# Kernel optimization log

Measured on AMD Instinct MI355X. Metric: run time of the kernel, lower is better.

## Reference

```python
import jax, jax.numpy as jnp
import numpy as np

B, F, T, D, W = 65536, 8, 60, 10, 6  # batch, features, time, window, n_windows
EPS = 1e-8
BN_EPS = 1e-5
IU, JU = np.triu_indices(F, k=1)  # 28 feature pairs


def _bn1d(x, g, b):
    # training-mode BatchNorm1d over [B, C, L]: stats over (B, L) per channel
    m = x.mean(axis=(0, 2), keepdims=True)
    v = x.var(axis=(0, 2), keepdims=True)
    return (x - m) * jax.lax.rsqrt(v + BN_EPS) * g[None, :, None] + b[None, :, None]


def setup_inputs() -> dict:
    key = jax.random.key(0)
    ks = jax.random.split(key, 8)
    s = 0.1
    return {
        "xb": jax.random.normal(ks[0], (B, 1, F, T), dtype=jnp.float32),
        "conv_w": jax.random.normal(ks[1], (4, 1, 1, D), dtype=jnp.float32) * s,
        "conv_b": jnp.zeros((4,), jnp.float32),
        "bn1_g": jnp.ones((28,), jnp.float32), "bn1_b": jnp.zeros((28,), jnp.float32),
        "bn4_g": jnp.ones((F,), jnp.float32), "bn4_b": jnp.zeros((F,), jnp.float32),
        "bn6_g": jnp.ones((F,), jnp.float32), "bn6_b": jnp.zeros((F,), jnp.float32),
        "bn9_g": jnp.ones((32,), jnp.float32), "bn9_b": jnp.zeros((32,), jnp.float32),
        "bnmax_g": jnp.ones((76,), jnp.float32), "bnmax_b": jnp.zeros((76,), jnp.float32),
        "w1": jax.random.normal(ks[2], (30, 608), dtype=jnp.float32) * s,
        "b1": jnp.zeros((30,), jnp.float32),
        "w2": jax.random.normal(ks[3], (1, 30), dtype=jnp.float32) * s,
        "b2": jnp.zeros((1,), jnp.float32),
    }


def reference(xb, conv_w, conv_b, bn1_g, bn1_b, bn4_g, bn4_b, bn6_g, bn6_b,
              bn9_g, bn9_b, bnmax_g, bnmax_b, w1, b1, w2, b2):
    b = xb.shape[0]
    xw = xb.reshape(b, F, W, D)  # non-overlapping windows of length D=10

    # ts_corr: pairwise Pearson correlation per window -> [b, 28, W]
    mu = xw.mean(axis=-1, keepdims=True)
    c = xw - mu
    cov = jnp.einsum('bfwt,bgwt->bfgw', c, c) / D          # [b,F,F,W]
    std = jnp.sqrt((c * c).mean(axis=-1) + EPS)            # [b,F,W]
    corr = cov / (std[:, :, None, :] * std[:, None, :, :] + EPS)
    xb1 = corr[:, IU, JU, :]                               # [b,28,W]

    # ts_zscore: mean/std per window -> [b, F, W]
    xb4 = mu[..., 0] / (std + EPS)

    # ts_decaylinear: linear-decay weighted mean -> [b, F, W]
    dw = jnp.arange(1, D + 1, dtype=jnp.float32)
    dw = dw / dw.sum()
    xb6 = jnp.einsum('bfwt,t->bfw', xw, dw)

    # conv2d kernel (1,10) stride (1,10) -> [b, 4*F, W]
    xb9 = jnp.einsum('bfwt,ot->bofw', xw, conv_w[:, 0, 0, :]) + conv_b[None, :, None, None]
    xb9 = xb9.reshape(b, 4 * F, W)

    h = jnp.concatenate([
        _bn1d(xb1, bn1_g, bn1_b),
        _bn1d(xb4, bn4_g, bn4_b),
        _bn1d(xb6, bn6_g, bn6_b),
        _bn1d(xb9, bn9_g, bn9_b),
    ], axis=1)                                             # [b,76,6]

    h_max = h.reshape(b, 76, 2, 3).max(axis=-1)            # MaxPool1d(3,3) -> [b,76,2]
    h_max = _bn1d(h_max, bnmax_g, bnmax_b)

    flat = jnp.concatenate([h.reshape(b, -1), h_max.reshape(b, -1)], axis=1)  # [b,608]
    out = jax.nn.relu(flat @ w1.T + b1) @ w2.T + b2
    return out.reshape(-1)
```

## Files before the change

kernel.cpp:

```cpp
#include <hip/hip_runtime.h>


#define NB 65536
#define EPS_F    1e-8f
#define BN_EPS_F 1e-5f

__device__ __forceinline__ float frcp(float x) {
  return __builtin_amdgcn_rcpf(x);
}

template<int Ctrl, int RowMask>
__device__ __forceinline__ float dpp_mov0(float v) {
  return __int_as_float(__builtin_amdgcn_update_dpp(
      0, __float_as_int(v), Ctrl, RowMask, 0xf, true));
}
__device__ __forceinline__ float wave_sum64(float v) {
  v += dpp_mov0<0x111, 0xf>(v);
  v += dpp_mov0<0x112, 0xf>(v);
  v += dpp_mov0<0x114, 0xf>(v);
  v += dpp_mov0<0x118, 0xf>(v);
  v += dpp_mov0<0x142, 0xa>(v);
  v += dpp_mov0<0x143, 0xc>(v);
  return v;
}

__host__ __device__ constexpr int UT(int i, int j) { return i*8 - i*(i-1)/2 + (j - i); }
__host__ __device__ constexpr int PIDX(int i, int j) { return i*7 - i*(i-1)/2 + (j - i - 1); }


__global__ void __launch_bounds__(256, 4)
k1f(const float* __restrict__ xb, const float* __restrict__ cw,
    const float* __restrict__ cb, float* __restrict__ F) {
  const int tid  = threadIdx.x;
  const int wave = tid >> 6, lane = tid & 63;
  const int role = __builtin_amdgcn_readfirstlane(wave);
  const int h    = role & 1;
  const int s    = blockIdx.x * 64 + lane;
  const float* xrow = xb + (size_t)s * 480 + h * 30;

  if (role < 2) {
    float mA[28];
    #pragma unroll
    for (int p = 0; p < 28; ++p) mA[p] = -3.0e38f;
    #pragma unroll
    for (int wl = 0; wl < 3; ++wl) {
      float sum[8], S[36];
      #pragma unroll
      for (int f = 0; f < 8; ++f) sum[f] = 0.f;
      #pragma unroll
      for (int k = 0; k < 36; ++k) S[k] = 0.f;
      #pragma unroll
      for (int tp = 0; tp < 5; ++tp) {
        float2 x2[8];
        #pragma unroll
        for (int f = 0; f < 8; ++f)
          x2[f] = *reinterpret_cast<const float2*>(xrow + f*60 + wl*10 + tp*2);
        #pragma unroll
        for (int f = 0; f < 8; ++f) sum[f] += x2[f].x + x2[f].y;
        #pragma unroll
        for (int i = 0; i < 8; ++i)
          #pragma unroll
          for (int j = i; j < 8; ++j)
            S[UT(i,j)] = fmaf(x2[i].y, x2[j].y, fmaf(x2[i].x, x2[j].x, S[UT(i,j)]));
      }
      float mu[8], sd[8];
      #pragma unroll
      for (int f = 0; f < 8; ++f) {
        mu[f] = sum[f] * 0.1f;
        sd[f] = sqrtf(fmaf(-mu[f], mu[f], S[UT(f,f)] * 0.1f) + EPS_F);
      }
      #pragma unroll
      for (int i = 0; i < 8; ++i)
        #pragma unroll
        for (int j = i + 1; j < 8; ++j) {
          float cov = fmaf(-mu[i], mu[j], S[UT(i,j)] * 0.1f);
          float v = cov * frcp(fmaf(sd[i], sd[j], EPS_F));
          int p = PIDX(i,j);
          F[(size_t)(p*6 + h*3 + wl) * NB + s] = v;
          mA[p] = fmaxf(mA[p], v);
        }
    }
    #pragma unroll
    for (int p = 0; p < 28; ++p)
      F[(size_t)(456 + p*2 + h) * NB + s] = mA[p];
  } else {
    #pragma unroll 1
    for (int f = 0; f < 8; ++f) {
      float m6[6];
      #pragma unroll
      for (int k = 0; k < 6; ++k) m6[k] = -3.0e38f;
      #pragma unroll
      for (int wl = 0; wl < 3; ++wl) {
        float2 x2[5];
        #pragma unroll
        for (int tp = 0; tp < 5; ++tp)
          x2[tp] = *reinterpret_cast<const float2*>(xrow + f*60 + wl*10 + tp*2);
        float sm = 0.f, sq = 0.f, wsm = 0.f;
        #pragma unroll
        for (int tp = 0; tp < 5; ++tp) {
          sm += x2[tp].x + x2[tp].y;
          sq = fmaf(x2[tp].x, x2[tp].x, fmaf(x2[tp].y, x2[tp].y, sq));
          wsm = fmaf(x2[tp].x, (float)(2*tp+1) * (1.f/55.f),
                fmaf(x2[tp].y, (float)(2*tp+2) * (1.f/55.f), wsm));
        }
        float mu = sm * 0.1f;
        float sd = sqrtf(fmaf(-mu, mu, sq * 0.1f) + EPS_F);
        float vv[6];
        vv[0] = mu * frcp(sd + EPS_F);
        vv[1] = wsm;
        #pragma unroll
        for (int o = 0; o < 4; ++o) {
          float cv = cb[o];
          #pragma unroll
          for (int tp = 0; tp < 5; ++tp)
            cv = fmaf(x2[tp].x, cw[o*10 + 2*tp], fmaf(x2[tp].y, cw[o*10 + 2*tp + 1], cv));
          vv[2+o] = cv;
        }
        #pragma unroll
        for (int k = 0; k < 6; ++k) {
          m6[k] = fmaxf(m6[k], vv[k]);
          int ch = (k == 0) ? (28 + f) : (k == 1) ? (36 + f) : (44 + (k-2)*8 + f);
          F[(size_t)(ch*6 + h*3 + wl) * NB + s] = vv[k];
        }
      }
      #pragma unroll
      for (int k = 0; k < 6; ++k) {
        int ch = (k == 0) ? (28 + f) : (k == 1) ? (36 + f) : (44 + (k-2)*8 + f);
        F[(size_t)(456 + ch*2 + h) * NB + s] = m6[k];
      }
    }
  }
}

__global__ void __launch_bounds__(256, 4)
kS(const float* __restrict__ F, float* __restrict__ stats) {
  const int r     = blockIdx.x >> 1;
  const int chunk = blockIdx.x & 1;
  const float* p  = F + (size_t)r * NB + chunk * 32768;
  const int tid = threadIdx.x;
  const int wave = tid >> 6, lane = tid & 63;
  float s = 0.f, q = 0.f;
  #pragma unroll 8
  for (int i = 0; i < 32; ++i) {
    float4 v = *reinterpret_cast<const float4*>(p + (size_t)(i*256 + tid) * 4);
    s += (v.x + v.y) + (v.z + v.w);
    q = fmaf(v.x, v.x, fmaf(v.y, v.y, fmaf(v.z, v.z, fmaf(v.w, v.w, q))));
  }
  s = wave_sum64(s);
  q = wave_sum64(q);
  __shared__ float ls[4], lq[4];
  if (lane == 63) { ls[wave] = s; lq[wave] = q; }
  __syncthreads();
  if (tid == 0) {
    float ts = (ls[0] + ls[1]) + (ls[2] + ls[3]);
    float tq = (lq[0] + lq[1]) + (lq[2] + lq[3]);
    int si, qi;
    if (r < 456) { int c = r / 6;        si = c;       qi = 76 + c;  }
    else         { int c = (r - 456)>>1; si = 152 + c; qi = 228 + c; }
    atomicAdd(&stats[si], ts);
    atomicAdd(&stats[qi], tq);
  }
}

__global__ void __launch_bounds__(256, 4)
k3f(const float* __restrict__ F, const float* __restrict__ w1s,
    const float* __restrict__ c0, const float* __restrict__ w2,
    const float* __restrict__ b2, float* __restrict__ out) {
  const int tid  = threadIdx.x;
  const int wave = tid >> 6, lane = tid & 63;
  const int kq   = __builtin_amdgcn_readfirstlane(wave);
  const int s    = blockIdx.x * 64 + lane;

  float a[30];
  #pragma unroll
  for (int j = 0; j < 30; ++j) a[j] = 0.f;

  const float* fp = F + (size_t)(kq * 152) * NB + s;
  #pragma unroll 8
  for (int r = 0; r < 152; ++r) {
    float v = fp[(size_t)r * NB];
    const float* wr = w1s + (kq * 152 + r) * 30;
    #pragma unroll
    for (int j = 0; j < 30; ++j) a[j] = fmaf(v, wr[j], a[j]);
  }

  __shared__ float accA[4][64][31];
  #pragma unroll
  for (int j = 0; j < 30; ++j) accA[wave][lane][j] = a[j];
  __syncthreads();
  if (wave == 0) {
    float t = b2[0];
    #pragma unroll
    for (int j = 0; j < 30; ++j) {
      float hj = ((accA[0][lane][j] + accA[1][lane][j]) +
                  (accA[2][lane][j] + accA[3][lane][j])) + c0[j];
      t = fmaf(w2[j], fmaxf(hj, 0.f), t);
    }
    out[blockIdx.x * 64 + lane] = t;
  }
}


__global__ void k2_params(const float* __restrict__ stats,
    const float* __restrict__ bn1g, const float* __restrict__ bn1b,
    const float* __restrict__ bn4g, const float* __restrict__ bn4b,
    const float* __restrict__ bn6g, const float* __restrict__ bn6b,
    const float* __restrict__ bn9g, const float* __restrict__ bn9b,
    const float* __restrict__ bnmg, const float* __restrict__ bnmb,
    float* __restrict__ params) {
  int c = threadIdx.x;
  if (c >= 76) return;
  float g, b;
  if      (c < 28) { g = bn1g[c];    b = bn1b[c];    }
  else if (c < 36) { g = bn4g[c-28]; b = bn4b[c-28]; }
  else if (c < 44) { g = bn6g[c-36]; b = bn6b[c-36]; }
  else             { g = bn9g[c-44]; b = bn9b[c-44]; }
  const float in1 = 1.0f / (65536.0f * 6.0f);
  const float in2 = 1.0f / (65536.0f * 2.0f);
  float mean = stats[c] * in1;
  float var  = stats[76 + c] * in1 - mean * mean;
  float r    = rsqrtf(var + BN_EPS_F);
  float sc1  = g * r;
  float sh1  = b - mean * sc1;
  float mmr  = stats[152 + c] * in2;
  float vmr  = stats[228 + c] * in2 - mmr * mmr;
  float meanm = sc1 * mmr + sh1;
  float varm  = sc1 * sc1 * vmr;
  float rm  = rsqrtf(varm + BN_EPS_F);
  float scm = bnmg[c] * rm;
  float shm = bnmb[c] - meanm * scm;
  params[c]        = sc1;
  params[76 + c]   = sh1;
  params[152 + c]  = scm;
  params[228 + c]  = shm;
}

__global__ void k2b(const float* __restrict__ w1, const float* __restrict__ params,
                    const float* __restrict__ b1, float* __restrict__ w1s,
                    float* __restrict__ c0) {
  int r = blockIdx.x;
  int j = threadIdx.x;
  float sc, cst;
  if (r < 456) {
    int c = r / 6;
    sc = params[c]; cst = params[76 + c];
  } else {
    int c = (r - 456) >> 1;
    float sc1 = params[c], sh1 = params[76 + c];
    float scm = params[152 + c], shm = params[228 + c];
    sc = sc1 * scm; cst = fmaf(scm, sh1, shm);
  }
  if (j < 30) {
    float w = w1[j * 608 + r];
    w1s[r * 30 + j] = sc * w;
    float cadd = cst * w;
    if (r == 0) cadd += b1[j];
    atomicAdd(&c0[j], cadd);
  }
}


__device__ __forceinline__ void flush4(float* acc, int ch, float s, float q,
                                       float m, bool ll) {
  float t0 = wave_sum64(s);
  float t1 = wave_sum64(q);
  float t2 = wave_sum64(m);
  float t3 = wave_sum64(m * m);
  if (ll) {
    atomicAdd(&acc[ch], t0);
    atomicAdd(&acc[76 + ch], t1);
    atomicAdd(&acc[152 + ch], t2);
    atomicAdd(&acc[228 + ch], t3);
  }
}

__global__ void __launch_bounds__(256, 2)
k1_stats(const float* __restrict__ xb, const float* __restrict__ cw,
         const float* __restrict__ cb, float* __restrict__ stats) {
  const int tid  = threadIdx.x;
  const int wave = tid >> 6, lane = tid & 63;
  const int half = __builtin_amdgcn_readfirstlane(wave & 1);
  const int sl   = (wave >> 1) * 64 + lane;
  const int sample = blockIdx.x * 128 + sl;
  const float* xrow = xb + (size_t)sample * 480 + half * 30;
  const bool ll = (lane == 63);

  __shared__ float acc[304];
  for (int i = tid; i < 304; i += 256) acc[i] = 0.f;
  __syncthreads();

  {
    float sA[28], qA[28], mA[28];
    #pragma unroll
    for (int p = 0; p < 28; ++p) { sA[p] = 0.f; qA[p] = 0.f; mA[p] = -3.0e38f; }
    #pragma unroll
    for (int wl = 0; wl < 3; ++wl) {
      float sum[8], S[36];
      #pragma unroll
      for (int f = 0; f < 8; ++f) sum[f] = 0.f;
      #pragma unroll
      for (int k = 0; k < 36; ++k) S[k] = 0.f;
      #pragma unroll
      for (int tp = 0; tp < 5; ++tp) {
        float2 x2[8];
        #pragma unroll
        for (int f = 0; f < 8; ++f)
          x2[f] = *reinterpret_cast<const float2*>(xrow + f*60 + wl*10 + tp*2);
        #pragma unroll
        for (int f = 0; f < 8; ++f) sum[f] += x2[f].x + x2[f].y;
        #pragma unroll
        for (int i = 0; i < 8; ++i)
          #pragma unroll
          for (int j = i; j < 8; ++j)
            S[UT(i,j)] = fmaf(x2[i].y, x2[j].y, fmaf(x2[i].x, x2[j].x, S[UT(i,j)]));
      }
      float mu[8], sd[8];
      #pragma unroll
      for (int f = 0; f < 8; ++f) {
        mu[f] = sum[f] * 0.1f;
        sd[f] = sqrtf(fmaf(-mu[f], mu[f], S[UT(f,f)] * 0.1f) + EPS_F);
      }
      #pragma unroll
      for (int i = 0; i < 8; ++i)
        #pragma unroll
        for (int j = i + 1; j < 8; ++j) {
          float cov = fmaf(-mu[i], mu[j], S[UT(i,j)] * 0.1f);
          float v = cov * frcp(fmaf(sd[i], sd[j], EPS_F));
          int p = PIDX(i,j);
          sA[p] += v; qA[p] = fmaf(v, v, qA[p]); mA[p] = fmaxf(mA[p], v);
        }
    }
    #pragma unroll
    for (int p = 0; p < 28; ++p) flush4(acc, p, sA[p], qA[p], mA[p], ll);
  }

  #pragma unroll 1
  for (int f = 0; f < 8; ++f) {
    float s6[6], q6[6], m6[6];
    #pragma unroll
    for (int k = 0; k < 6; ++k) { s6[k] = 0.f; q6[k] = 0.f; m6[k] = -3.0e38f; }
    #pragma unroll
    for (int wl = 0; wl < 3; ++wl) {
      float2 x2[5];
      #pragma unroll
      for (int tp = 0; tp < 5; ++tp)
        x2[tp] = *reinterpret_cast<const float2*>(xrow + f*60 + wl*10 + tp*2);
      float sm = 0.f, sq = 0.f, wsm = 0.f;
      #pragma unroll
      for (int tp = 0; tp < 5; ++tp) {
        sm += x2[tp].x + x2[tp].y;
        sq = fmaf(x2[tp].x, x2[tp].x, fmaf(x2[tp].y, x2[tp].y, sq));
        wsm = fmaf(x2[tp].x, (float)(2*tp+1) * (1.f/55.f),
              fmaf(x2[tp].y, (float)(2*tp+2) * (1.f/55.f), wsm));
      }
      float mu = sm * 0.1f;
      float sd = sqrtf(fmaf(-mu, mu, sq * 0.1f) + EPS_F);
      float v0 = mu * frcp(sd + EPS_F);
      s6[0] += v0; q6[0] = fmaf(v0, v0, q6[0]); m6[0] = fmaxf(m6[0], v0);
      s6[1] += wsm; q6[1] = fmaf(wsm, wsm, q6[1]); m6[1] = fmaxf(m6[1], wsm);
      #pragma unroll
      for (int o = 0; o < 4; ++o) {
        float cv = cb[o];
        #pragma unroll
        for (int tp = 0; tp < 5; ++tp)
          cv = fmaf(x2[tp].x, cw[o*10 + 2*tp], fmaf(x2[tp].y, cw[o*10 + 2*tp + 1], cv));
        s6[2+o] += cv; q6[2+o] = fmaf(cv, cv, q6[2+o]); m6[2+o] = fmaxf(m6[2+o], cv);
      }
    }
    flush4(acc, 28 + f, s6[0], q6[0], m6[0], ll);
    flush4(acc, 36 + f, s6[1], q6[1], m6[1], ll);
    #pragma unroll
    for (int o = 0; o < 4; ++o)
      flush4(acc, 44 + o*8 + f, s6[2+o], q6[2+o], m6[2+o], ll);
  }

  __syncthreads();
  for (int i = tid; i < 304; i += 256) atomicAdd(&stats[i], acc[i]);
}

__global__ void __launch_bounds__(256, 2)
k3_out(const float* __restrict__ xb, const float* __restrict__ cw,
       const float* __restrict__ cb, const float* __restrict__ w1s,
       const float* __restrict__ c0, const float* __restrict__ w2,
       const float* __restrict__ b2, float* __restrict__ out) {
  const int tid  = threadIdx.x;
  const int wave = tid >> 6, lane = tid & 63;
  const int half = __builtin_amdgcn_readfirstlane(wave & 1);
  const int sl   = (wave >> 1) * 64 + lane;
  const int sample = blockIdx.x * 128 + sl;
  const float* xrow = xb + (size_t)sample * 480 + half * 30;

  float a[30];
  #pragma unroll
  for (int j = 0; j < 30; ++j) a[j] = 0.f;

  {
    float mA[28];
    #pragma unroll
    for (int p = 0; p < 28; ++p) mA[p] = -3.0e38f;
    #pragma unroll
    for (int wl = 0; wl < 3; ++wl) {
      float sum[8], S[36];
      #pragma unroll
      for (int f = 0; f < 8; ++f) sum[f] = 0.f;
      #pragma unroll
      for (int k = 0; k < 36; ++k) S[k] = 0.f;
      #pragma unroll
      for (int tp = 0; tp < 5; ++tp) {
        float2 x2[8];
        #pragma unroll
        for (int f = 0; f < 8; ++f)
          x2[f] = *reinterpret_cast<const float2*>(xrow + f*60 + wl*10 + tp*2);
        #pragma unroll
        for (int f = 0; f < 8; ++f) sum[f] += x2[f].x + x2[f].y;
        #pragma unroll
        for (int i = 0; i < 8; ++i)
          #pragma unroll
          for (int j = i; j < 8; ++j)
            S[UT(i,j)] = fmaf(x2[i].y, x2[j].y, fmaf(x2[i].x, x2[j].x, S[UT(i,j)]));
      }
      float mu[8], sd[8];
      #pragma unroll
      for (int f = 0; f < 8; ++f) {
        mu[f] = sum[f] * 0.1f;
        sd[f] = sqrtf(fmaf(-mu[f], mu[f], S[UT(f,f)] * 0.1f) + EPS_F);
      }
      #pragma unroll
      for (int i = 0; i < 8; ++i)
        #pragma unroll
        for (int j = i + 1; j < 8; ++j) {
          float cov = fmaf(-mu[i], mu[j], S[UT(i,j)] * 0.1f);
          float v = cov * frcp(fmaf(sd[i], sd[j], EPS_F));
          int p = PIDX(i,j);
          mA[p] = fmaxf(mA[p], v);
          const float* wr = w1s + (p*6 + half*3 + wl) * 30;
          #pragma unroll
          for (int j2 = 0; j2 < 30; ++j2) a[j2] = fmaf(v, wr[j2], a[j2]);
        }
    }
    #pragma unroll
    for (int p = 0; p < 28; ++p) {
      const float* wr = w1s + (456 + p*2 + half) * 30;
      #pragma unroll
      for (int j2 = 0; j2 < 30; ++j2) a[j2] = fmaf(mA[p], wr[j2], a[j2]);
    }
  }

  #pragma unroll 1
  for (int f = 0; f < 8; ++f) {
    float m6[6];
    #pragma unroll
    for (int k = 0; k < 6; ++k) m6[k] = -3.0e38f;
    #pragma unroll
    for (int wl = 0; wl < 3; ++wl) {
      float2 x2[5];
      #pragma unroll
      for (int tp = 0; tp < 5; ++tp)
        x2[tp] = *reinterpret_cast<const float2*>(xrow + f*60 + wl*10 + tp*2);
      float sm = 0.f, sq = 0.f, wsm = 0.f;
      #pragma unroll
      for (int tp = 0; tp < 5; ++tp) {
        sm += x2[tp].x + x2[tp].y;
        sq = fmaf(x2[tp].x, x2[tp].x, fmaf(x2[tp].y, x2[tp].y, sq));
        wsm = fmaf(x2[tp].x, (float)(2*tp+1) * (1.f/55.f),
              fmaf(x2[tp].y, (float)(2*tp+2) * (1.f/55.f), wsm));
      }
      float mu = sm * 0.1f;
      float sd = sqrtf(fmaf(-mu, mu, sq * 0.1f) + EPS_F);
      float vv[6];
      vv[0] = mu * frcp(sd + EPS_F);
      vv[1] = wsm;
      #pragma unroll
      for (int o = 0; o < 4; ++o) {
        float cv = cb[o];
        #pragma unroll
        for (int tp = 0; tp < 5; ++tp)
          cv = fmaf(x2[tp].x, cw[o*10 + 2*tp], fmaf(x2[tp].y, cw[o*10 + 2*tp + 1], cv));
        vv[2+o] = cv;
      }
      #pragma unroll
      for (int k = 0; k < 6; ++k) {
        m6[k] = fmaxf(m6[k], vv[k]);
        int ch = (k == 0) ? (28 + f) : (k == 1) ? (36 + f) : (44 + (k-2)*8 + f);
        const float* wr = w1s + (ch*6 + half*3 + wl) * 30;
        #pragma unroll
        for (int j2 = 0; j2 < 30; ++j2) a[j2] = fmaf(vv[k], wr[j2], a[j2]);
      }
    }
    #pragma unroll
    for (int k = 0; k < 6; ++k) {
      int ch = (k == 0) ? (28 + f) : (k == 1) ? (36 + f) : (44 + (k-2)*8 + f);
      const float* wr = w1s + (456 + ch*2 + half) * 30;
      #pragma unroll
      for (int j2 = 0; j2 < 30; ++j2) a[j2] = fmaf(m6[k], wr[j2], a[j2]);
    }
  }

  __shared__ float accA[128][31];
  if (half == 0) {
    #pragma unroll
    for (int j = 0; j < 30; ++j) accA[sl][j] = a[j];
  }
  __syncthreads();
  if (half == 1) {
    #pragma unroll
    for (int j = 0; j < 30; ++j) accA[sl][j] += a[j];
  }
  __syncthreads();
  if (tid < 128) {
    float t = b2[0];
    #pragma unroll
    for (int j = 0; j < 30; ++j)
      t = fmaf(w2[j], fmaxf(accA[tid][j] + c0[j], 0.f), t);
    out[blockIdx.x * 128 + tid] = t;
  }
}


extern "C" void kernel_launch(void* const* d_in, const int* in_sizes, int n_in,
                              void* d_out, int out_size, void* d_ws, size_t ws_size,
                              hipStream_t stream) {
  (void)in_sizes; (void)n_in; (void)out_size;
  const float* xb   = (const float*)d_in[0];
  const float* cw   = (const float*)d_in[1];
  const float* cb   = (const float*)d_in[2];
  const float* bn1g = (const float*)d_in[3];
  const float* bn1b = (const float*)d_in[4];
  const float* bn4g = (const float*)d_in[5];
  const float* bn4b = (const float*)d_in[6];
  const float* bn6g = (const float*)d_in[7];
  const float* bn6b = (const float*)d_in[8];
  const float* bn9g = (const float*)d_in[9];
  const float* bn9b = (const float*)d_in[10];
  const float* bnmg = (const float*)d_in[11];
  const float* bnmb = (const float*)d_in[12];
  const float* w1   = (const float*)d_in[13];
  const float* b1   = (const float*)d_in[14];
  const float* w2   = (const float*)d_in[15];
  const float* b2   = (const float*)d_in[16];

  float* out    = (float*)d_out;
  float* ws     = (float*)d_ws;
  float* stats  = ws;
  float* params = ws + 304;
  float* c0     = ws + 608;
  float* w1s    = ws + 640;
  float* F      = ws + 18880;

  const size_t needed = ((size_t)18880 + (size_t)608 * NB) * sizeof(float);

  hipMemsetAsync(ws, 0, 640 * sizeof(float), stream);
  if (ws_size >= needed) {
    k1f<<<1024, 256, 0, stream>>>(xb, cw, cb, F);
    kS<<<1216, 256, 0, stream>>>(F, stats);
    k2_params<<<1, 128, 0, stream>>>(stats, bn1g, bn1b, bn4g, bn4b, bn6g, bn6b,
                                     bn9g, bn9b, bnmg, bnmb, params);
    k2b<<<608, 64, 0, stream>>>(w1, params, b1, w1s, c0);
    k3f<<<1024, 256, 0, stream>>>(F, w1s, c0, w2, b2, out);
  } else {
    k1_stats<<<512, 256, 0, stream>>>(xb, cw, cb, stats);
    k2_params<<<1, 128, 0, stream>>>(stats, bn1g, bn1b, bn4g, bn4b, bn6g, bn6b,
                                     bn9g, bn9b, bnmg, bnmb, params);
    k2b<<<608, 64, 0, stream>>>(w1, params, b1, w1s, c0);
    k3_out<<<512, 256, 0, stream>>>(xb, cw, cb, w1s, c0, w2, b2, out);
  }
}
```

Before: 381.6 us.

## Replace materialized feature buffer with two-pass recompute kernels staging input in LDS

Removes the 608×B intermediate feature tensor and its separate stats-reduction kernel. Instead it runs one templated kernel twice: a first pass that recomputes features and accumulates BN statistics with wave reductions and atomics, and a second pass that recomputes features and applies the folded linear layer directly. Input tiles are loaded coalesced into LDS in two halves with register prefetch, and work is split across waves by feature groups. This trades DRAM traffic for duplicated feature computation and higher LDS and register usage.

```diff
diff --git a/kernel.cpp b/kernel.cpp
--- a/kernel.cpp
+++ b/kernel.cpp
@@ -4,6 +4,7 @@
 #define NB 65536
 #define EPS_F    1e-8f
 #define BN_EPS_F 1e-5f
+#define LDSW 242
 
 __device__ __forceinline__ float frcp(float x) {
   return __builtin_amdgcn_rcpf(x);
@@ -24,179 +25,282 @@
   return v;
 }
 
-__host__ __device__ constexpr int UT(int i, int j) { return i*8 - i*(i-1)/2 + (j - i); }
-__host__ __device__ constexpr int PIDX(int i, int j) { return i*7 - i*(i-1)/2 + (j - i - 1); }
-
-
-__global__ void __launch_bounds__(256, 4)
-k1f(const float* __restrict__ xb, const float* __restrict__ cw,
-    const float* __restrict__ cb, float* __restrict__ F) {
-  const int tid  = threadIdx.x;
-  const int wave = tid >> 6, lane = tid & 63;
-  const int role = __builtin_amdgcn_readfirstlane(wave);
-  const int h    = role & 1;
-  const int s    = blockIdx.x * 64 + lane;
-  const float* xrow = xb + (size_t)s * 480 + h * 30;
-
-  if (role < 2) {
-    float mA[28];
-    #pragma unroll
-    for (int p = 0; p < 28; ++p) mA[p] = -3.0e38f;
+constexpr int PI_[28] = {0,0,0,0,0,0,0, 1,1,1,1,1,1, 2,2,2,2,2, 3,3,3,3, 4,4,4, 5,5, 6};
+constexpr int PJ_[28] = {1,2,3,4,5,6,7, 2,3,4,5,6,7, 3,4,5,6,7, 4,5,6,7, 5,6,7, 6,7, 7};
+
+template<int PASS, int W>
+__device__ __forceinline__ void corr_wave(
+    const float* __restrict__ bx, const int h,
+    const float* __restrict__ w1s,
+    float* __restrict__ sacc, float* __restrict__ qacc,
+    float* __restrict__ msacc, float* __restrict__ m2acc,
+    float* __restrict__ a)
+{
+  constexpr int PLO = W * 14;
+  constexpr int FLO = W * 4;
+  float m[18];
+  #pragma unroll
+  for (int k = 0; k < 18; ++k) m[k] = -3.0e38f;
+
+  #pragma unroll
+  for (int wl = 0; wl < 3; ++wl) {
+    float sum[8], SD[8], SP[14];
+    #pragma unroll
+    for (int f = 0; f < 8; ++f) { sum[f] = 0.f; SD[f] = 0.f; }
+    #pragma unroll
+    for (int k = 0; k < 14; ++k) SP[k] = 0.f;
+    #pragma unroll
+    for (int tp = 0; tp < 5; ++tp) {
+      float2 x2[8];
+      #pragma unroll
+      for (int f = 0; f < 8; ++f)
+        x2[f] = *reinterpret_cast<const float2*>(bx + f*30 + wl*10 + tp*2);
+      #pragma unroll
+      for (int f = 0; f < 8; ++f) {
+        sum[f] += x2[f].x + x2[f].y;
+        SD[f] = fmaf(x2[f].x, x2[f].x, fmaf(x2[f].y, x2[f].y, SD[f]));
+      }
+      #pragma unroll
+      for (int k = 0; k < 14; ++k) {
+        const int i = PI_[PLO + k], j = PJ_[PLO + k];
+        SP[k] = fmaf(x2[i].x, x2[j].x, fmaf(x2[i].y, x2[j].y, SP[k]));
+      }
+    }
+    float mu[8], sd[8];
+    #pragma unroll
+    for (int f = 0; f < 8; ++f) {
+      mu[f] = sum[f] * 0.1f;
+      sd[f] = sqrtf(fmaf(-mu[f], mu[f], SD[f] * 0.1f) + EPS_F);
+    }
+    #pragma unroll
+    for (int k = 0; k < 14; ++k) {
+      const int i = PI_[PLO + k], j = PJ_[PLO + k];
+      float cov = fmaf(-mu[i], mu[j], SP[k] * 0.1f);
+      float v = cov * frcp(fmaf(sd[i], sd[j], EPS_F));
+      m[k] = fmaxf(m[k], v);
+      if (PASS == 0) {
+        sacc[k] += v; qacc[k] = fmaf(v, v, qacc[k]);
+      } else {
+        const float* wr = w1s + ((PLO + k)*6 + h*3 + wl) * 30;
+        #pragma unroll
+        for (int j2 = 0; j2 < 30; ++j2) a[j2] = fmaf(v, wr[j2], a[j2]);
+      }
+    }
+    #pragma unroll
+    for (int q = 0; q < 4; ++q) {
+      const int f = FLO + q, k = 14 + q;
+      float v = mu[f] * frcp(sd[f] + EPS_F);
+      m[k] = fmaxf(m[k], v);
+      if (PASS == 0) {
+        sacc[k] += v; qacc[k] = fmaf(v, v, qacc[k]);
+      } else {
+        const float* wr = w1s + ((28 + f)*6 + h*3 + wl) * 30;
+        #pragma unroll
+        for (int j2 = 0; j2 < 30; ++j2) a[j2] = fmaf(v, wr[j2], a[j2]);
+      }
+    }
+  }
+  #pragma unroll
+  for (int k = 0; k < 18; ++k) {
+    const int ch = (k < 14) ? (PLO + k) : (28 + FLO + (k - 14));
+    if (PASS == 0) {
+      msacc[k] += m[k]; m2acc[k] = fmaf(m[k], m[k], m2acc[k]);
+    } else {
+      const float* wr = w1s + (456 + ch*2 + h) * 30;
+      #pragma unroll
+      for (int j2 = 0; j2 < 30; ++j2) a[j2] = fmaf(m[k], wr[j2], a[j2]);
+    }
+  }
+}
+
+template<int PASS, int G>
+__device__ __forceinline__ void bc_wave(
+    const float* __restrict__ bx, const int h,
+    const float* __restrict__ cw, const float* __restrict__ cb,
+    const float* __restrict__ w1s,
+    float* __restrict__ sacc, float* __restrict__ qacc,
+    float* __restrict__ msacc, float* __restrict__ m2acc,
+    float* __restrict__ a)
+{
+  constexpr int FLO = G * 4;
+  float m[20];
+  #pragma unroll
+  for (int k = 0; k < 20; ++k) m[k] = -3.0e38f;
+
+  #pragma unroll
+  for (int q = 0; q < 4; ++q) {
+    const int f = FLO + q;
     #pragma unroll
     for (int wl = 0; wl < 3; ++wl) {
-      float sum[8], S[36];
-      #pragma unroll
-      for (int f = 0; f < 8; ++f) sum[f] = 0.f;
-      #pragma unroll
-      for (int k = 0; k < 36; ++k) S[k] = 0.f;
-      #pragma unroll
-      for (int tp = 0; tp < 5; ++tp) {
-        float2 x2[8];
-        #pragma unroll
-        for (int f = 0; f < 8; ++f)
-          x2[f] = *reinterpret_cast<const float2*>(xrow + f*60 + wl*10 + tp*2);
-        #pragma unroll
-        for (int f = 0; f < 8; ++f) sum[f] += x2[f].x + x2[f].y;
-        #pragma unroll
-        for (int i = 0; i < 8; ++i)
+      float2 x2[5];
+      #pragma unroll
+      for (int tp = 0; tp < 5; ++tp)
+        x2[tp] = *reinterpret_cast<const float2*>(bx + f*30 + wl*10 + tp*2);
+      float wsm = 0.f;
+      #pragma unroll
+      for (int tp = 0; tp < 5; ++tp)
+        wsm = fmaf(x2[tp].x, (float)(2*tp+1) * (1.f/55.f),
+              fmaf(x2[tp].y, (float)(2*tp+2) * (1.f/55.f), wsm));
+      {
+        const int k = q*5;
+        m[k] = fmaxf(m[k], wsm);
+        if (PASS == 0) { sacc[k] += wsm; qacc[k] = fmaf(wsm, wsm, qacc[k]); }
+        else {
+          const float* wr = w1s + ((36 + f)*6 + h*3 + wl) * 30;
           #pragma unroll
-          for (int j = i; j < 8; ++j)
-            S[UT(i,j)] = fmaf(x2[i].y, x2[j].y, fmaf(x2[i].x, x2[j].x, S[UT(i,j)]));
-      }
-      float mu[8], sd[8];
-      #pragma unroll
-      for (int f = 0; f < 8; ++f) {
-        mu[f] = sum[f] * 0.1f;
-        sd[f] = sqrtf(fmaf(-mu[f], mu[f], S[UT(f,f)] * 0.1f) + EPS_F);
-      }
-      #pragma unroll
-      for (int i = 0; i < 8; ++i)
-        #pragma unroll
-        for (int j = i + 1; j < 8; ++j) {
-          float cov = fmaf(-mu[i], mu[j], S[UT(i,j)] * 0.1f);
-          float v = cov * frcp(fmaf(sd[i], sd[j], EPS_F));
-          int p = PIDX(i,j);
-          F[(size_t)(p*6 + h*3 + wl) * NB + s] = v;
-          mA[p] = fmaxf(mA[p], v);
+          for (int j2 = 0; j2 < 30; ++j2) a[j2] = fmaf(wsm, wr[j2], a[j2]);
         }
-    }
-    #pragma unroll
-    for (int p = 0; p < 28; ++p)
-      F[(size_t)(456 + p*2 + h) * NB + s] = mA[p];
-  } else {
-    #pragma unroll 1
-    for (int f = 0; f < 8; ++f) {
-      float m6[6];
-      #pragma unroll
-      for (int k = 0; k < 6; ++k) m6[k] = -3.0e38f;
-      #pragma unroll
-      for (int wl = 0; wl < 3; ++wl) {
-        float2 x2[5];
+      }
+      #pragma unroll
+      for (int o = 0; o < 4; ++o) {
+        float cv = cb[o];
         #pragma unroll
         for (int tp = 0; tp < 5; ++tp)
-          x2[tp] = *reinterpret_cast<const float2*>(xrow + f*60 + wl*10 + tp*2);
-        float sm = 0.f, sq = 0.f, wsm = 0.f;
-        #pragma unroll
-        for (int tp = 0; tp < 5; ++tp) {
-          sm += x2[tp].x + x2[tp].y;
-          sq = fmaf(x2[tp].x, x2[tp].x, fmaf(x2[tp].y, x2[tp].y, sq));
-          wsm = fmaf(x2[tp].x, (float)(2*tp+1) * (1.f/55.f),
-                fmaf(x2[tp].y, (float)(2*tp+2) * (1.f/55.f), wsm));
+          cv = fmaf(x2[tp].x, cw[o*10 + 2*tp], fmaf(x2[tp].y, cw[o*10 + 2*tp + 1], cv));
+        const int k = q*5 + 1 + o;
+        m[k] = fmaxf(m[k], cv);
+        if (PASS == 0) { sacc[k] += cv; qacc[k] = fmaf(cv, cv, qacc[k]); }
+        else {
+          const float* wr = w1s + ((44 + o*8 + f)*6 + h*3 + wl) * 30;
+          #pragma unroll
+          for (int j2 = 0; j2 < 30; ++j2) a[j2] = fmaf(cv, wr[j2], a[j2]);
         }
-        float mu = sm * 0.1f;
-        float sd = sqrtf(fmaf(-mu, mu, sq * 0.1f) + EPS_F);
-        float vv[6];
-        vv[0] = mu * frcp(sd + EPS_F);
-        vv[1] = wsm;
-        #pragma unroll
-        for (int o = 0; o < 4; ++o) {
-          float cv = cb[o];
-          #pragma unroll
-          for (int tp = 0; tp < 5; ++tp)
-            cv = fmaf(x2[tp].x, cw[o*10 + 2*tp], fmaf(x2[tp].y, cw[o*10 + 2*tp + 1], cv));
-          vv[2+o] = cv;
+      }
+    }
+  }
+  #pragma unroll
+  for (int k = 0; k < 20; ++k) {
+    const int f = FLO + k/5, c = k%5;
+    const int ch = (c == 0) ? (36 + f) : (44 + (c-1)*8 + f);
+    if (PASS == 0) {
+      msacc[k] += m[k]; m2acc[k] = fmaf(m[k], m[k], m2acc[k]);
+    } else {
+      const float* wr = w1s + (456 + ch*2 + h) * 30;
+      #pragma unroll
+      for (int j2 = 0; j2 < 30; ++j2) a[j2] = fmaf(m[k], wr[j2], a[j2]);
+    }
+  }
+}
+
+template<int PASS>
+__global__ void __launch_bounds__(256, 2)
+alpha_pass(const float* __restrict__ xb, const float* __restrict__ cw,
+           const float* __restrict__ cb, const float* __restrict__ w1s,
+           const float* __restrict__ c0, const float* __restrict__ w2,
+           const float* __restrict__ b2, float* __restrict__ stats,
+           float* __restrict__ out)
+{
+  __shared__ float sx[64 * LDSW];
+  const int tid  = threadIdx.x;
+  const int wave = __builtin_amdgcn_readfirstlane(threadIdx.x >> 6);
+  const int lane = tid & 63;
+
+  float sacc[20], qacc[20], msacc[20], m2acc[20];
+  float a[30];
+  if (PASS == 0) {
+    #pragma unroll
+    for (int k = 0; k < 20; ++k) { sacc[k]=0.f; qacc[k]=0.f; msacc[k]=0.f; m2acc[k]=0.f; }
+  } else {
+    #pragma unroll
+    for (int j = 0; j < 30; ++j) a[j] = 0.f;
+  }
+
+  const float* gb = xb + (size_t)blockIdx.x * (64 * 480);
+  float2 pf[30];
+
+  #pragma unroll
+  for (int k = 0; k < 30; ++k) {
+    const int i  = k * 256 + tid;
+    const int sm = i / 120;
+    const int r  = i - sm * 120;
+    const int f  = r / 15;
+    const int c  = r - f * 15;
+    pf[k] = *reinterpret_cast<const float2*>(gb + sm*480 + f*60 + c*2);
+  }
+  #pragma unroll
+  for (int k = 0; k < 30; ++k) {
+    const int i  = k * 256 + tid;
+    const int sm = i / 120;
+    const int r  = i - sm * 120;
+    const int f  = r / 15;
+    const int c  = r - f * 15;
+    *reinterpret_cast<float2*>(sx + sm*LDSW + f*30 + c*2) = pf[k];
+  }
+  __syncthreads();
+
+  #pragma unroll
+  for (int k = 0; k < 30; ++k) {
+    const int i  = k * 256 + tid;
+    const int sm = i / 120;
+    const int r  = i - sm * 120;
+    const int f  = r / 15;
+    const int c  = r - f * 15;
+    pf[k] = *reinterpret_cast<const float2*>(gb + sm*480 + f*60 + 30 + c*2);
+  }
+
+  const float* bx = sx + lane * LDSW;
+
+  if      (wave == 0) corr_wave<PASS,0>(bx, 0, w1s, sacc,qacc,msacc,m2acc, a);
+  else if (wave == 1) corr_wave<PASS,1>(bx, 0, w1s, sacc,qacc,msacc,m2acc, a);
+  else if (wave == 2) bc_wave<PASS,0>(bx, 0, cw, cb, w1s, sacc,qacc,msacc,m2acc, a);
+  else                bc_wave<PASS,1>(bx, 0, cw, cb, w1s, sacc,qacc,msacc,m2acc, a);
+  __syncthreads();
+
+  #pragma unroll
+  for (int k = 0; k < 30; ++k) {
+    const int i  = k * 256 + tid;
+    const int sm = i / 120;
+    const int r  = i - sm * 120;
+    const int f  = r / 15;
+    const int c  = r - f * 15;
+    *reinterpret_cast<float2*>(sx + sm*LDSW + f*30 + c*2) = pf[k];
+  }
+  __syncthreads();
+
+  if      (wave == 0) corr_wave<PASS,0>(bx, 1, w1s, sacc,qacc,msacc,m2acc, a);
+  else if (wave == 1) corr_wave<PASS,1>(bx, 1, w1s, sacc,qacc,msacc,m2acc, a);
+  else if (wave == 2) bc_wave<PASS,0>(bx, 1, cw, cb, w1s, sacc,qacc,msacc,m2acc, a);
+  else                bc_wave<PASS,1>(bx, 1, cw, cb, w1s, sacc,qacc,msacc,m2acc, a);
+
+  if (PASS == 0) {
+    const int nch = (wave < 2) ? 18 : 20;
+    #pragma unroll
+    for (int k = 0; k < 20; ++k) {
+      if (k < nch) {
+        float t0 = wave_sum64(sacc[k]);
+        float t1 = wave_sum64(qacc[k]);
+        float t2 = wave_sum64(msacc[k]);
+        float t3 = wave_sum64(m2acc[k]);
+        int ch;
+        if (wave < 2) {
+          ch = (k < 14) ? (wave*14 + k) : (28 + wave*4 + (k - 14));
+        } else {
+          const int f = (wave - 2)*4 + k/5, c = k%5;
+          ch = (c == 0) ? (36 + f) : (44 + (c-1)*8 + f);
         }
-        #pragma unroll
-        for (int k = 0; k < 6; ++k) {
-          m6[k] = fmaxf(m6[k], vv[k]);
-          int ch = (k == 0) ? (28 + f) : (k == 1) ? (36 + f) : (44 + (k-2)*8 + f);
-          F[(size_t)(ch*6 + h*3 + wl) * NB + s] = vv[k];
+        if (lane == 63) {
+          atomicAdd(&stats[ch],       t0);
+          atomicAdd(&stats[76 + ch],  t1);
+          atomicAdd(&stats[152 + ch], t2);
+          atomicAdd(&stats[228 + ch], t3);
         }
       }
-      #pragma unroll
-      for (int k = 0; k < 6; ++k) {
-        int ch = (k == 0) ? (28 + f) : (k == 1) ? (36 + f) : (44 + (k-2)*8 + f);
-        F[(size_t)(456 + ch*2 + h) * NB + s] = m6[k];
-      }
-    }
-  }
-}
-
-__global__ void __launch_bounds__(256, 4)
-kS(const float* __restrict__ F, float* __restrict__ stats) {
-  const int r     = blockIdx.x >> 1;
-  const int chunk = blockIdx.x & 1;
-  const float* p  = F + (size_t)r * NB + chunk * 32768;
-  const int tid = threadIdx.x;
-  const int wave = tid >> 6, lane = tid & 63;
-  float s = 0.f, q = 0.f;
-  #pragma unroll 8
-  for (int i = 0; i < 32; ++i) {
-    float4 v = *reinterpret_cast<const float4*>(p + (size_t)(i*256 + tid) * 4);
-    s += (v.x + v.y) + (v.z + v.w);
-    q = fmaf(v.x, v.x, fmaf(v.y, v.y, fmaf(v.z, v.z, fmaf(v.w, v.w, q))));
-  }
-  s = wave_sum64(s);
-  q = wave_sum64(q);
-  __shared__ float ls[4], lq[4];
-  if (lane == 63) { ls[wave] = s; lq[wave] = q; }
-  __syncthreads();
-  if (tid == 0) {
-    float ts = (ls[0] + ls[1]) + (ls[2] + ls[3]);
-    float tq = (lq[0] + lq[1]) + (lq[2] + lq[3]);
-    int si, qi;
-    if (r < 456) { int c = r / 6;        si = c;       qi = 76 + c;  }
-    else         { int c = (r - 456)>>1; si = 152 + c; qi = 228 + c; }
-    atomicAdd(&stats[si], ts);
-    atomicAdd(&stats[qi], tq);
-  }
-}
-
-__global__ void __launch_bounds__(256, 4)
-k3f(const float* __restrict__ F, const float* __restrict__ w1s,
-    const float* __restrict__ c0, const float* __restrict__ w2,
-    const float* __restrict__ b2, float* __restrict__ out) {
-  const int tid  = threadIdx.x;
-  const int wave = tid >> 6, lane = tid & 63;
-  const int kq   = __builtin_amdgcn_readfirstlane(wave);
-  const int s    = blockIdx.x * 64 + lane;
-
-  float a[30];
-  #pragma unroll
-  for (int j = 0; j < 30; ++j) a[j] = 0.f;
-
-  const float* fp = F + (size_t)(kq * 152) * NB + s;
-  #pragma unroll 8
-  for (int r = 0; r < 152; ++r) {
-    float v = fp[(size_t)r * NB];
-    const float* wr = w1s + (kq * 152 + r) * 30;
-    #pragma unroll
-    for (int j = 0; j < 30; ++j) a[j] = fmaf(v, wr[j], a[j]);
-  }
-
-  __shared__ float accA[4][64][31];
-  #pragma unroll
-  for (int j = 0; j < 30; ++j) accA[wave][lane][j] = a[j];
-  __syncthreads();
-  if (wave == 0) {
-    float t = b2[0];
-    #pragma unroll
-    for (int j = 0; j < 30; ++j) {
-      float hj = ((accA[0][lane][j] + accA[1][lane][j]) +
-                  (accA[2][lane][j] + accA[3][lane][j])) + c0[j];
-      t = fmaf(w2[j], fmaxf(hj, 0.f), t);
-    }
-    out[blockIdx.x * 64 + lane] = t;
+    }
+  } else {
+    __syncthreads();
+    #pragma unroll
+    for (int j = 0; j < 30; ++j) sx[tid*31 + j] = a[j];
+    __syncthreads();
+    if (tid < 64) {
+      float t = b2[0];
+      #pragma unroll
+      for (int j = 0; j < 30; ++j) {
+        float hh = ((sx[tid*31 + j] + sx[(64 + tid)*31 + j]) +
+                    (sx[(128 + tid)*31 + j] + sx[(192 + tid)*31 + j])) + c0[j];
+        t = fmaf(w2[j], fmaxf(hh, 0.f), t);
+      }
+      out[blockIdx.x * 64 + tid] = t;
+    }
   }
 }
 
@@ -260,267 +364,10 @@
 }
 
 
-__device__ __forceinline__ void flush4(float* acc, int ch, float s, float q,
-                                       float m, bool ll) {
-  float t0 = wave_sum64(s);
-  float t1 = wave_sum64(q);
-  float t2 = wave_sum64(m);
-  float t3 = wave_sum64(m * m);
-  if (ll) {
-    atomicAdd(&acc[ch], t0);
-    atomicAdd(&acc[76 + ch], t1);
-    atomicAdd(&acc[152 + ch], t2);
-    atomicAdd(&acc[228 + ch], t3);
-  }
-}
-
-__global__ void __launch_bounds__(256, 2)
-k1_stats(const float* __restrict__ xb, const float* __restrict__ cw,
-         const float* __restrict__ cb, float* __restrict__ stats) {
-  const int tid  = threadIdx.x;
-  const int wave = tid >> 6, lane = tid & 63;
-  const int half = __builtin_amdgcn_readfirstlane(wave & 1);
-  const int sl   = (wave >> 1) * 64 + lane;
-  const int sample = blockIdx.x * 128 + sl;
-  const float* xrow = xb + (size_t)sample * 480 + half * 30;
-  const bool ll = (lane == 63);
-
-  __shared__ float acc[304];
-  for (int i = tid; i < 304; i += 256) acc[i] = 0.f;
-  __syncthreads();
-
-  {
-    float sA[28], qA[28], mA[28];
-    #pragma unroll
-    for (int p = 0; p < 28; ++p) { sA[p] = 0.f; qA[p] = 0.f; mA[p] = -3.0e38f; }
-    #pragma unroll
-    for (int wl = 0; wl < 3; ++wl) {
-      float sum[8], S[36];
-      #pragma unroll
-      for (int f = 0; f < 8; ++f) sum[f] = 0.f;
-      #pragma unroll
-      for (int k = 0; k < 36; ++k) S[k] = 0.f;
-      #pragma unroll
-      for (int tp = 0; tp < 5; ++tp) {
-        float2 x2[8];
-        #pragma unroll
-        for (int f = 0; f < 8; ++f)
-          x2[f] = *reinterpret_cast<const float2*>(xrow + f*60 + wl*10 + tp*2);
-        #pragma unroll
-        for (int f = 0; f < 8; ++f) sum[f] += x2[f].x + x2[f].y;
-        #pragma unroll
-        for (int i = 0; i < 8; ++i)
-          #pragma unroll
-          for (int j = i; j < 8; ++j)
-            S[UT(i,j)] = fmaf(x2[i].y, x2[j].y, fmaf(x2[i].x, x2[j].x, S[UT(i,j)]));
-      }
-      float mu[8], sd[8];
-      #pragma unroll
-      for (int f = 0; f < 8; ++f) {
-        mu[f] = sum[f] * 0.1f;
-        sd[f] = sqrtf(fmaf(-mu[f], mu[f], S[UT(f,f)] * 0.1f) + EPS_F);
-      }
-      #pragma unroll
-      for (int i = 0; i < 8; ++i)
-        #pragma unroll
-        for (int j = i + 1; j < 8; ++j) {
-          float cov = fmaf(-mu[i], mu[j], S[UT(i,j)] * 0.1f);
-          float v = cov * frcp(fmaf(sd[i], sd[j], EPS_F));
-          int p = PIDX(i,j);
-          sA[p] += v; qA[p] = fmaf(v, v, qA[p]); mA[p] = fmaxf(mA[p], v);
-        }
-    }
-    #pragma unroll
-    for (int p = 0; p < 28; ++p) flush4(acc, p, sA[p], qA[p], mA[p], ll);
-  }
-
-  #pragma unroll 1
-  for (int f = 0; f < 8; ++f) {
-    float s6[6], q6[6], m6[6];
-    #pragma unroll
-    for (int k = 0; k < 6; ++k) { s6[k] = 0.f; q6[k] = 0.f; m6[k] = -3.0e38f; }
-    #pragma unroll
-    for (int wl = 0; wl < 3; ++wl) {
-      float2 x2[5];
-      #pragma unroll
-      for (int tp = 0; tp < 5; ++tp)
-        x2[tp] = *reinterpret_cast<const float2*>(xrow + f*60 + wl*10 + tp*2);
-      float sm = 0.f, sq = 0.f, wsm = 0.f;
-      #pragma unroll
-      for (int tp = 0; tp < 5; ++tp) {
-        sm += x2[tp].x + x2[tp].y;
-        sq = fmaf(x2[tp].x, x2[tp].x, fmaf(x2[tp].y, x2[tp].y, sq));
-        wsm = fmaf(x2[tp].x, (float)(2*tp+1) * (1.f/55.f),
-              fmaf(x2[tp].y, (float)(2*tp+2) * (1.f/55.f), wsm));
-      }
-      float mu = sm * 0.1f;
-      float sd = sqrtf(fmaf(-mu, mu, sq * 0.1f) + EPS_F);
-      float v0 = mu * frcp(sd + EPS_F);
-      s6[0] += v0; q6[0] = fmaf(v0, v0, q6[0]); m6[0] = fmaxf(m6[0], v0);
-      s6[1] += wsm; q6[1] = fmaf(wsm, wsm, q6[1]); m6[1] = fmaxf(m6[1], wsm);
-      #pragma unroll
-      for (int o = 0; o < 4; ++o) {
-        float cv = cb[o];
-        #pragma unroll
-        for (int tp = 0; tp < 5; ++tp)
-          cv = fmaf(x2[tp].x, cw[o*10 + 2*tp], fmaf(x2[tp].y, cw[o*10 + 2*tp + 1], cv));
-        s6[2+o] += cv; q6[2+o] = fmaf(cv, cv, q6[2+o]); m6[2+o] = fmaxf(m6[2+o], cv);
-      }
-    }
-    flush4(acc, 28 + f, s6[0], q6[0], m6[0], ll);
-    flush4(acc, 36 + f, s6[1], q6[1], m6[1], ll);
-    #pragma unroll
-    for (int o = 0; o < 4; ++o)
-      flush4(acc, 44 + o*8 + f, s6[2+o], q6[2+o], m6[2+o], ll);
-  }
-
-  __syncthreads();
-  for (int i = tid; i < 304; i += 256) atomicAdd(&stats[i], acc[i]);
-}
-
-__global__ void __launch_bounds__(256, 2)
-k3_out(const float* __restrict__ xb, const float* __restrict__ cw,
-       const float* __restrict__ cb, const float* __restrict__ w1s,
-       const float* __restrict__ c0, const float* __restrict__ w2,
-       const float* __restrict__ b2, float* __restrict__ out) {
-  const int tid  = threadIdx.x;
-  const int wave = tid >> 6, lane = tid & 63;
-  const int half = __builtin_amdgcn_readfirstlane(wave & 1);
-  const int sl   = (wave >> 1) * 64 + lane;
-  const int sample = blockIdx.x * 128 + sl;
-  const float* xrow = xb + (size_t)sample * 480 + half * 30;
-
-  float a[30];
-  #pragma unroll
-  for (int j = 0; j < 30; ++j) a[j] = 0.f;
-
-  {
-    float mA[28];
-    #pragma unroll
-    for (int p = 0; p < 28; ++p) mA[p] = -3.0e38f;
-    #pragma unroll
-    for (int wl = 0; wl < 3; ++wl) {
-      float sum[8], S[36];
-      #pragma unroll
-      for (int f = 0; f < 8; ++f) sum[f] = 0.f;
-      #pragma unroll
-      for (int k = 0; k < 36; ++k) S[k] = 0.f;
-      #pragma unroll
-      for (int tp = 0; tp < 5; ++tp) {
-        float2 x2[8];
-        #pragma unroll
-        for (int f = 0; f < 8; ++f)
-          x2[f] = *reinterpret_cast<const float2*>(xrow + f*60 + wl*10 + tp*2);
-        #pragma unroll
-        for (int f = 0; f < 8; ++f) sum[f] += x2[f].x + x2[f].y;
-        #pragma unroll
-        for (int i = 0; i < 8; ++i)
-          #pragma unroll
-          for (int j = i; j < 8; ++j)
-            S[UT(i,j)] = fmaf(x2[i].y, x2[j].y, fmaf(x2[i].x, x2[j].x, S[UT(i,j)]));
-      }
-      float mu[8], sd[8];
-      #pragma unroll
-      for (int f = 0; f < 8; ++f) {
-        mu[f] = sum[f] * 0.1f;
-        sd[f] = sqrtf(fmaf(-mu[f], mu[f], S[UT(f,f)] * 0.1f) + EPS_F);
-      }
-      #pragma unroll
-      for (int i = 0; i < 8; ++i)
-        #pragma unroll
-        for (int j = i + 1; j < 8; ++j) {
-          float cov = fmaf(-mu[i], mu[j], S[UT(i,j)] * 0.1f);
-          float v = cov * frcp(fmaf(sd[i], sd[j], EPS_F));
-          int p = PIDX(i,j);
-          mA[p] = fmaxf(mA[p], v);
-          const float* wr = w1s + (p*6 + half*3 + wl) * 30;
-          #pragma unroll
-          for (int j2 = 0; j2 < 30; ++j2) a[j2] = fmaf(v, wr[j2], a[j2]);
-        }
-    }
-    #pragma unroll
-    for (int p = 0; p < 28; ++p) {
-      const float* wr = w1s + (456 + p*2 + half) * 30;
-      #pragma unroll
-      for (int j2 = 0; j2 < 30; ++j2) a[j2] = fmaf(mA[p], wr[j2], a[j2]);
-    }
-  }
-
-  #pragma unroll 1
-  for (int f = 0; f < 8; ++f) {
-    float m6[6];
-    #pragma unroll
-    for (int k = 0; k < 6; ++k) m6[k] = -3.0e38f;
-    #pragma unroll
-    for (int wl = 0; wl < 3; ++wl) {
-      float2 x2[5];
-      #pragma unroll
-      for (int tp = 0; tp < 5; ++tp)
-        x2[tp] = *reinterpret_cast<const float2*>(xrow + f*60 + wl*10 + tp*2);
-      float sm = 0.f, sq = 0.f, wsm = 0.f;
-      #pragma unroll
-      for (int tp = 0; tp < 5; ++tp) {
-        sm += x2[tp].x + x2[tp].y;
-        sq = fmaf(x2[tp].x, x2[tp].x, fmaf(x2[tp].y, x2[tp].y, sq));
-        wsm = fmaf(x2[tp].x, (float)(2*tp+1) * (1.f/55.f),
-              fmaf(x2[tp].y, (float)(2*tp+2) * (1.f/55.f), wsm));
-      }
-      float mu = sm * 0.1f;
-      float sd = sqrtf(fmaf(-mu, mu, sq * 0.1f) + EPS_F);
-      float vv[6];
-      vv[0] = mu * frcp(sd + EPS_F);
-      vv[1] = wsm;
-      #pragma unroll
-      for (int o = 0; o < 4; ++o) {
-        float cv = cb[o];
-        #pragma unroll
-        for (int tp = 0; tp < 5; ++tp)
-          cv = fmaf(x2[tp].x, cw[o*10 + 2*tp], fmaf(x2[tp].y, cw[o*10 + 2*tp + 1], cv));
-        vv[2+o] = cv;
-      }
-      #pragma unroll
-      for (int k = 0; k < 6; ++k) {
-        m6[k] = fmaxf(m6[k], vv[k]);
-        int ch = (k == 0) ? (28 + f) : (k == 1) ? (36 + f) : (44 + (k-2)*8 + f);
-        const float* wr = w1s + (ch*6 + half*3 + wl) * 30;
-        #pragma unroll
-        for (int j2 = 0; j2 < 30; ++j2) a[j2] = fmaf(vv[k], wr[j2], a[j2]);
-      }
-    }
-    #pragma unroll
-    for (int k = 0; k < 6; ++k) {
-      int ch = (k == 0) ? (28 + f) : (k == 1) ? (36 + f) : (44 + (k-2)*8 + f);
-      const float* wr = w1s + (456 + ch*2 + half) * 30;
-      #pragma unroll
-      for (int j2 = 0; j2 < 30; ++j2) a[j2] = fmaf(m6[k], wr[j2], a[j2]);
-    }
-  }
-
-  __shared__ float accA[128][31];
-  if (half == 0) {
-    #pragma unroll
-    for (int j = 0; j < 30; ++j) accA[sl][j] = a[j];
-  }
-  __syncthreads();
-  if (half == 1) {
-    #pragma unroll
-    for (int j = 0; j < 30; ++j) accA[sl][j] += a[j];
-  }
-  __syncthreads();
-  if (tid < 128) {
-    float t = b2[0];
-    #pragma unroll
-    for (int j = 0; j < 30; ++j)
-      t = fmaf(w2[j], fmaxf(accA[tid][j] + c0[j], 0.f), t);
-    out[blockIdx.x * 128 + tid] = t;
-  }
-}
-
-
 extern "C" void kernel_launch(void* const* d_in, const int* in_sizes, int n_in,
                               void* d_out, int out_size, void* d_ws, size_t ws_size,
                               hipStream_t stream) {
-  (void)in_sizes; (void)n_in; (void)out_size;
+  (void)in_sizes; (void)n_in; (void)out_size; (void)ws_size;
   const float* xb   = (const float*)d_in[0];
   const float* cw   = (const float*)d_in[1];
   const float* cb   = (const float*)d_in[2];
@@ -532,12 +379,12 @@
   const float* bn6b = (const float*)d_in[8];
   const float* bn9g = (const float*)d_in[9];
   const float* bn9b = (const float*)d_in[10];
-  const float* bnmg = (const float*)d_in[11];
-  const float* bnmb = (const float*)d_in[12];
   const float* w1   = (const float*)d_in[13];
   const float* b1   = (const float*)d_in[14];
   const float* w2   = (const float*)d_in[15];
   const float* b2   = (const float*)d_in[16];
+  const float* bnmg = (const float*)d_in[11];
+  const float* bnmb = (const float*)d_in[12];
 
   float* out    = (float*)d_out;
   float* ws     = (float*)d_ws;
@@ -545,23 +392,13 @@
   float* params = ws + 304;
   float* c0     = ws + 608;
   float* w1s    = ws + 640;
-  float* F      = ws + 18880;
-
-  const size_t needed = ((size_t)18880 + (size_t)608 * NB) * sizeof(float);
 
   hipMemsetAsync(ws, 0, 640 * sizeof(float), stream);
-  if (ws_size >= needed) {
-    k1f<<<1024, 256, 0, stream>>>(xb, cw, cb, F);
-    kS<<<1216, 256, 0, stream>>>(F, stats);
-    k2_params<<<1, 128, 0, stream>>>(stats, bn1g, bn1b, bn4g, bn4b, bn6g, bn6b,
-                                     bn9g, bn9b, bnmg, bnmb, params);
-    k2b<<<608, 64, 0, stream>>>(w1, params, b1, w1s, c0);
-    k3f<<<1024, 256, 0, stream>>>(F, w1s, c0, w2, b2, out);
-  } else {
-    k1_stats<<<512, 256, 0, stream>>>(xb, cw, cb, stats);
-    k2_params<<<1, 128, 0, stream>>>(stats, bn1g, bn1b, bn4g, bn4b, bn6g, bn6b,
-                                     bn9g, bn9b, bnmg, bnmb, params);
-    k2b<<<608, 64, 0, stream>>>(w1, params, b1, w1s, c0);
-    k3_out<<<512, 256, 0, stream>>>(xb, cw, cb, w1s, c0, w2, b2, out);
-  }
-}
+  alpha_pass<0><<<1024, 256, 0, stream>>>(xb, cw, cb, nullptr, nullptr, nullptr,
+                                          nullptr, stats, nullptr);
+  k2_params<<<1, 128, 0, stream>>>(stats, bn1g, bn1b, bn4g, bn4b, bn6g, bn6b,
+                                   bn9g, bn9b, bnmg, bnmb, params);
+  k2b<<<608, 64, 0, stream>>>(w1, params, b1, w1s, c0);
+  alpha_pass<1><<<1024, 256, 0, stream>>>(xb, cw, cb, w1s, c0, w2, b2,
+                                          nullptr, out);
+}
```

New measurement: 876.8 us. +129.8%, slower.
